# Kernel tuning notes

Measured on AMD Instinct MI355X. Metric: run time of the kernel, lower is better.

Reference implementation:

```python
import jax, jax.numpy as jnp
import numpy as np

DN = jax.lax.conv_dimension_numbers((1, 32, 32, 32, 1), (3, 3, 3, 1, 32), ('NDHWC', 'DHWIO', 'NDHWC'))


def setup_inputs() -> dict:
    key = jax.random.key(0)
    k0, k1, k2, k3, k4 = jax.random.split(key, 5)
    B = 64
    x = jax.random.normal(k0, (B, 32, 32, 32, 1), dtype=jnp.float32)
    # conv weights in DHWIO layout; kaiming-ish scale
    w1 = jax.random.normal(k1, (3, 3, 3, 1, 32), dtype=jnp.float32) * (1.0 / np.sqrt(27 * 1))
    b1 = jax.random.normal(k2, (32,), dtype=jnp.float32) * 0.01
    w2 = jax.random.normal(k3, (3, 3, 3, 32, 64), dtype=jnp.float32) * (1.0 / np.sqrt(27 * 32))
    b2 = jax.random.normal(k4, (64,), dtype=jnp.float32) * 0.01
    return {"x": x, "w1": w1, "b1": b1, "w2": w2, "b2": b2}


def _conv3d_valid(x, w):
    # x: [B, D, H, W, C_in], w: [kD, kH, kW, C_in, C_out] -> [B, D-2, H-2, W-2, C_out]
    dn = jax.lax.conv_dimension_numbers(x.shape, w.shape, ('NDHWC', 'DHWIO', 'NDHWC'))
    return jax.lax.conv_general_dilated(x, w, window_strides=(1, 1, 1),
                                        padding='VALID', dimension_numbers=dn)


def reference(x, w1, b1, w2, b2):
    # Dense input -> all voxels active, so spconv's gather-GEMM-scatter equals
    # a dense valid 3D conv. ReLU acts on active-site features == dense ReLU.
    h = jax.nn.relu(_conv3d_valid(x, w1) + b1)        # [B, 30, 30, 30, 32]
    h = jax.nn.relu(_conv3d_valid(h, w2) + b2)        # [B, 28, 28, 28, 64]
    # spconv ToDense returns NCDHW
    return jnp.transpose(h, (0, 4, 1, 2, 3))          # [B, 64, 28, 28, 28]
```

## Files before the change

kernel.cpp:

```cpp
#include <hip/hip_runtime.h>
#include <cstdint>
#include <cstddef>

typedef __attribute__((ext_vector_type(8))) short bf16x8;
typedef __attribute__((ext_vector_type(4))) float f32x4;
typedef __attribute__((ext_vector_type(4))) unsigned int u32x4;
typedef unsigned short u16;

#define H1_ROW_B   1920
#define H1_BATCH   (30 * 30 * 960)
#define LDS_STRIDE 1952
#define OUT_CSTR   21952

__device__ __forceinline__ u16 f2bf(float f) {
    union { float f; unsigned u; } v; v.f = f;
    unsigned r = v.u + 0x7FFF + ((v.u >> 16) & 1);
    return (u16)(r >> 16);
}

__device__ __forceinline__ void fma4(float4& a, float s, const float4& w) {
    a.x = fmaf(s, w.x, a.x);
    a.y = fmaf(s, w.y, a.y);
    a.z = fmaf(s, w.z, a.z);
    a.w = fmaf(s, w.w, a.w);
}

__global__ __launch_bounds__(256) void conv1_relu(
    const float* __restrict__ x, const float* __restrict__ w1,
    const float* __restrict__ b1, u16* __restrict__ h1, int b0)
{
    __shared__ float wl[27 * 32 + 32];

    const int z   = blockIdx.x;
    const int yt  = blockIdx.y;
    const int bl  = blockIdx.z;
    const int b   = b0 + bl;
    const int tid = threadIdx.x;

    for (int i = tid; i < 27 * 32; i += 256) wl[i] = w1[i];
    if (tid < 32) wl[27 * 32 + tid] = b1[tid];
    __syncthreads();

    const int c4   = tid & 7;
    const int slot = tid >> 3;

    const float4 bias = *reinterpret_cast<const float4*>(&wl[27 * 32 + c4 * 4]);
    const float* xb  = x + (size_t)b * 32768;
    u16*         h1b = h1 + (size_t)bl * H1_BATCH;

    if (slot < 30) {
#pragma unroll 1
        for (int j = 0; j < 3; ++j) {
            const int p  = slot + 30 * j;
            const int yy = p / 15;
            const int xx = (p - yy * 15) * 2;
            const int y  = yt * 6 + yy;

            float4 acc0 = bias, acc1 = bias;
#pragma unroll
            for (int kd = 0; kd < 3; ++kd) {
#pragma unroll
                for (int kh = 0; kh < 3; ++kh) {
                    const float* row = xb + ((size_t)(z + kd) * 32 + (y + kh)) * 32 + xx;
                    const float2 v01 = *reinterpret_cast<const float2*>(row);
                    const float2 v23 = *reinterpret_cast<const float2*>(row + 2);
                    const int t = (kd * 3 + kh) * 3;
                    const float4 w0  = *reinterpret_cast<const float4*>(&wl[(t + 0) * 32 + c4 * 4]);
                    const float4 w1v = *reinterpret_cast<const float4*>(&wl[(t + 1) * 32 + c4 * 4]);
                    const float4 w2v = *reinterpret_cast<const float4*>(&wl[(t + 2) * 32 + c4 * 4]);
                    fma4(acc0, v01.x, w0);
                    fma4(acc0, v01.y, w1v);
                    fma4(acc0, v23.x, w2v);
                    fma4(acc1, v01.y, w0);
                    fma4(acc1, v23.x, w1v);
                    fma4(acc1, v23.y, w2v);
                }
            }
            ushort4 s0, s1;
            s0.x = f2bf(fmaxf(acc0.x, 0.f)); s0.y = f2bf(fmaxf(acc0.y, 0.f));
            s0.z = f2bf(fmaxf(acc0.z, 0.f)); s0.w = f2bf(fmaxf(acc0.w, 0.f));
            s1.x = f2bf(fmaxf(acc1.x, 0.f)); s1.y = f2bf(fmaxf(acc1.y, 0.f));
            s1.z = f2bf(fmaxf(acc1.z, 0.f)); s1.w = f2bf(fmaxf(acc1.w, 0.f));
            u16* dst = h1b + ((size_t)(z * 30 + y) * 30 + xx) * 32 + c4 * 4;
            *reinterpret_cast<ushort4*>(dst)      = s0;
            *reinterpret_cast<ushort4*>(dst + 32) = s1;
        }
    }
}

__global__ __launch_bounds__(256) void pack_w2(
    const float* __restrict__ w2, u16* __restrict__ wB)
{
    const int tap = blockIdx.x;
    const int tid = threadIdx.x;
    const int nt = tid >> 6;
    const int l  = tid & 63;
    const int r = l & 15, q = l >> 4;
    u16* dst = wB + ((size_t)(tap * 4 + nt) * 64 + l) * 8;
#pragma unroll
    for (int j = 0; j < 8; ++j)
        dst[j] = f2bf(w2[(size_t)(tap * 32 + q * 8 + j) * 64 + nt * 16 + r]);
}

__global__ __launch_bounds__(256, 2) void conv2_mfma(
    const u16* __restrict__ h1, const u16* __restrict__ wB,
    const float* __restrict__ b2, float* __restrict__ out, int b0)
{
    __shared__ __align__(16) unsigned char smem[36 * LDS_STRIDE];

    const int g   = gridDim.x;
    const int bid = blockIdx.x;
    const int lb  = (g % 8 == 0) ? ((bid & 7) * (g >> 3) + (bid >> 3)) : bid;

    const int t0  = lb % 49;
    const int bl  = lb / 49;
    const int yg  = t0 % 7;
    const int zt  = t0 / 7;

    const int b  = b0 + bl;
    const int y0 = yg * 4, z0 = zt * 4;
    const int tid = threadIdx.x;
    const int wv  = tid >> 6;
    const int l   = tid & 63;
    const int r = l & 15, q = l >> 4;
    const int yl = r >> 2, xg = r & 3;

    const char* wBl = (const char*)wB + l * 16;

    {
        const char* gbase = (const char*)(h1 + (size_t)bl * H1_BATCH);
        for (int c = wv; c < 72; c += 4) {
            const int rid = c >> 1, half = c & 1;
            const int zz = rid / 6, yy = rid - zz * 6;
            const char* src = gbase
                + (size_t)((z0 + zz) * 30 + (y0 + yy)) * H1_ROW_B
                + half * 896 + l * 16;
            unsigned char* dst = smem + rid * LDS_STRIDE + half * 896 + l * 16;
            __builtin_amdgcn_global_load_lds(
                (const __attribute__((address_space(1))) void*)src,
                (__attribute__((address_space(3))) void*)dst, 16, 0, 0);
        }
    }
    __syncthreads();

    f32x4 acc[7][4];
    {
        const float bv0 = b2[r];
        const float bv1 = b2[16 + r];
        const float bv2 = b2[32 + r];
        const float bv3 = b2[48 + r];
#pragma unroll
        for (int mt = 0; mt < 7; ++mt) {
            acc[mt][0] = (f32x4){bv0, bv0, bv0, bv0};
            acc[mt][1] = (f32x4){bv1, bv1, bv1, bv1};
            acc[mt][2] = (f32x4){bv2, bv2, bv2, bv2};
            acc[mt][3] = (f32x4){bv3, bv3, bv3, bv3};
        }
    }

    const unsigned char* aBase =
        smem + (wv * 6 + yl) * LDS_STRIDE + xg * 64 + q * 16;

    u32x4 Bs[2][4];
#define B_LOAD(slot, t)                                                        \
    { const char* p_ = wBl + (size_t)(t) * 4096;                               \
      asm volatile("global_load_dwordx4 %0, %4, off\n\t"                       \
                   "global_load_dwordx4 %1, %4, off offset:1024\n\t"           \
                   "global_load_dwordx4 %2, %4, off offset:2048\n\t"           \
                   "global_load_dwordx4 %3, %4, off offset:3072"               \
                   : "=&v"(Bs[slot][0]), "=&v"(Bs[slot][1]),                   \
                     "=&v"(Bs[slot][2]), "=&v"(Bs[slot][3])                    \
                   : "v"(p_)); }

    B_LOAD(0, 0)

#pragma unroll
    for (int tap = 0; tap < 27; ++tap) {
        const int cur = tap & 1;

        if (tap < 26) B_LOAD(cur ^ 1, tap + 1)

        if (tap < 26) asm volatile("s_waitcnt vmcnt(4)");
        else          asm volatile("s_waitcnt vmcnt(0)");

        asm volatile("" : "+v"(Bs[cur][0]), "+v"(Bs[cur][1]),
                          "+v"(Bs[cur][2]), "+v"(Bs[cur][3]));
        const bf16x8 B0 = __builtin_bit_cast(bf16x8, Bs[cur][0]);
        const bf16x8 B1 = __builtin_bit_cast(bf16x8, Bs[cur][1]);
        const bf16x8 B2 = __builtin_bit_cast(bf16x8, Bs[cur][2]);
        const bf16x8 B3 = __builtin_bit_cast(bf16x8, Bs[cur][3]);

        const int kd = tap / 9;
        const int kh = (tap - kd * 9) / 3;
        const int kw = tap - kd * 9 - kh * 3;
        const unsigned char* ap = aBase + (kd * 6 + kh) * LDS_STRIDE + kw * 64;

        __builtin_amdgcn_s_setprio(1);
#pragma unroll
        for (int mt = 0; mt < 7; ++mt) {
            const bf16x8 a = *reinterpret_cast<const bf16x8*>(ap + mt * 256);
            acc[mt][0] = __builtin_amdgcn_mfma_f32_16x16x32_bf16(a, B0, acc[mt][0], 0, 0, 0);
            acc[mt][1] = __builtin_amdgcn_mfma_f32_16x16x32_bf16(a, B1, acc[mt][1], 0, 0, 0);
            acc[mt][2] = __builtin_amdgcn_mfma_f32_16x16x32_bf16(a, B2, acc[mt][2], 0, 0, 0);
            acc[mt][3] = __builtin_amdgcn_mfma_f32_16x16x32_bf16(a, B3, acc[mt][3], 0, 0, 0);
        }
        __builtin_amdgcn_s_setprio(0);
    }
#undef B_LOAD

    const int z = z0 + wv;
    float* ob = out + ((size_t)b * 64 + r) * OUT_CSTR
                    + (size_t)z * 784 + (size_t)(y0 + q) * 28;
#pragma unroll
    for (int mt = 0; mt < 7; ++mt) {
#pragma unroll
        for (int nt = 0; nt < 4; ++nt) {
            const f32x4 v = acc[mt][nt];
            float4 st;
            st.x = fmaxf(v.x, 0.f);
            st.y = fmaxf(v.y, 0.f);
            st.z = fmaxf(v.z, 0.f);
            st.w = fmaxf(v.w, 0.f);
            *reinterpret_cast<float4*>(ob + (size_t)nt * 16 * OUT_CSTR + mt * 4) = st;
        }
    }
}

extern "C" void kernel_launch(void* const* d_in, const int* in_sizes, int n_in,
                              void* d_out, int out_size, void* d_ws, size_t ws_size,
                              hipStream_t stream)
{
    const float* x  = (const float*)d_in[0];
    const float* w1 = (const float*)d_in[1];
    const float* b1 = (const float*)d_in[2];
    const float* w2 = (const float*)d_in[3];
    const float* b2 = (const float*)d_in[4];
    float* out = (float*)d_out;

    u16* wB = (u16*)d_ws;
    u16* h1 = (u16*)((char*)d_ws + 131072);

    pack_w2<<<27, 256, 0, stream>>>(w2, wB);

    const size_t per_batch = (size_t)H1_BATCH * 2;
    size_t avail = ws_size > 131072 ? ws_size - 131072 : 0;
    int bchunk = (int)(avail / per_batch);
    if (bchunk < 1)  bchunk = 1;
    if (bchunk > 64) bchunk = 64;

    for (int b0 = 0; b0 < 64; b0 += bchunk) {
        int bc = 64 - b0;
        if (bc > bchunk) bc = bchunk;
        conv1_relu<<<dim3(30, 5, bc), 256, 0, stream>>>(x, w1, b1, h1, b0);
        conv2_mfma<<<dim3(49 * bc), 256, 0, stream>>>(h1, wB, b2, out, b0);
    }
}
```

Measured before the change: 295.5 us.

## Split conv2 x-range across two waves per z-slice with 512-thread blocks

The conv2 MFMA kernel moves from 4 waves to 8 waves per block. Each z-slice's 7 M-tiles are now split between two waves, one taking 4 tiles and the other 3, with the compute body templated on tile count and x offset. The aim is more waves per block for better latency hiding and fewer accumulator registers per wave. In exchange, every B-weight load is duplicated across twice as many waves, and the two halves carry unequal work.

```diff
diff --git a/kernel.cpp b/kernel.cpp
--- a/kernel.cpp
+++ b/kernel.cpp
@@ -102,64 +102,26 @@
         dst[j] = f2bf(w2[(size_t)(tap * 32 + q * 8 + j) * 64 + nt * 16 + r]);
 }
 
-__global__ __launch_bounds__(256, 2) void conv2_mfma(
-    const u16* __restrict__ h1, const u16* __restrict__ wB,
-    const float* __restrict__ b2, float* __restrict__ out, int b0)
-{
-    __shared__ __align__(16) unsigned char smem[36 * LDS_STRIDE];
-
-    const int g   = gridDim.x;
-    const int bid = blockIdx.x;
-    const int lb  = (g % 8 == 0) ? ((bid & 7) * (g >> 3) + (bid >> 3)) : bid;
-
-    const int t0  = lb % 49;
-    const int bl  = lb / 49;
-    const int yg  = t0 % 7;
-    const int zt  = t0 / 7;
-
-    const int b  = b0 + bl;
-    const int y0 = yg * 4, z0 = zt * 4;
-    const int tid = threadIdx.x;
-    const int wv  = tid >> 6;
-    const int l   = tid & 63;
+template<int NMT, int XOUT>
+__device__ __forceinline__ void conv2_body(
+    const unsigned char* smem, const char* wBl,
+    const float* __restrict__ b2, float* __restrict__ out,
+    int b, int y0, int z0, int zw, int l)
+{
     const int r = l & 15, q = l >> 4;
     const int yl = r >> 2, xg = r & 3;
 
-    const char* wBl = (const char*)wB + l * 16;
-
-    {
-        const char* gbase = (const char*)(h1 + (size_t)bl * H1_BATCH);
-        for (int c = wv; c < 72; c += 4) {
-            const int rid = c >> 1, half = c & 1;
-            const int zz = rid / 6, yy = rid - zz * 6;
-            const char* src = gbase
-                + (size_t)((z0 + zz) * 30 + (y0 + yy)) * H1_ROW_B
-                + half * 896 + l * 16;
-            unsigned char* dst = smem + rid * LDS_STRIDE + half * 896 + l * 16;
-            __builtin_amdgcn_global_load_lds(
-                (const __attribute__((address_space(1))) void*)src,
-                (__attribute__((address_space(3))) void*)dst, 16, 0, 0);
-        }
-    }
-    __syncthreads();
-
-    f32x4 acc[7][4];
-    {
-        const float bv0 = b2[r];
-        const float bv1 = b2[16 + r];
-        const float bv2 = b2[32 + r];
-        const float bv3 = b2[48 + r];
-#pragma unroll
-        for (int mt = 0; mt < 7; ++mt) {
-            acc[mt][0] = (f32x4){bv0, bv0, bv0, bv0};
-            acc[mt][1] = (f32x4){bv1, bv1, bv1, bv1};
-            acc[mt][2] = (f32x4){bv2, bv2, bv2, bv2};
-            acc[mt][3] = (f32x4){bv3, bv3, bv3, bv3};
-        }
+    f32x4 acc[NMT][4];
+#pragma unroll
+    for (int nt = 0; nt < 4; ++nt) {
+        const float bv = b2[nt * 16 + r];
+        const f32x4 bi = {bv, bv, bv, bv};
+#pragma unroll
+        for (int mt = 0; mt < NMT; ++mt) acc[mt][nt] = bi;
     }
 
     const unsigned char* aBase =
-        smem + (wv * 6 + yl) * LDS_STRIDE + xg * 64 + q * 16;
+        smem + (zw * 6 + yl) * LDS_STRIDE + (XOUT + xg) * 64 + q * 16;
 
     u32x4 Bs[2][4];
 #define B_LOAD(slot, t)                                                        \
@@ -197,7 +159,7 @@
 
         __builtin_amdgcn_s_setprio(1);
 #pragma unroll
-        for (int mt = 0; mt < 7; ++mt) {
+        for (int mt = 0; mt < NMT; ++mt) {
             const bf16x8 a = *reinterpret_cast<const bf16x8*>(ap + mt * 256);
             acc[mt][0] = __builtin_amdgcn_mfma_f32_16x16x32_bf16(a, B0, acc[mt][0], 0, 0, 0);
             acc[mt][1] = __builtin_amdgcn_mfma_f32_16x16x32_bf16(a, B1, acc[mt][1], 0, 0, 0);
@@ -208,11 +170,11 @@
     }
 #undef B_LOAD
 
-    const int z = z0 + wv;
+    const int z = z0 + zw;
     float* ob = out + ((size_t)b * 64 + r) * OUT_CSTR
-                    + (size_t)z * 784 + (size_t)(y0 + q) * 28;
-#pragma unroll
-    for (int mt = 0; mt < 7; ++mt) {
+                    + (size_t)z * 784 + (size_t)(y0 + q) * 28 + XOUT;
+#pragma unroll
+    for (int mt = 0; mt < NMT; ++mt) {
 #pragma unroll
         for (int nt = 0; nt < 4; ++nt) {
             const f32x4 v = acc[mt][nt];
@@ -226,6 +188,53 @@
     }
 }
 
+__global__ __launch_bounds__(512, 4) void conv2_mfma(
+    const u16* __restrict__ h1, const u16* __restrict__ wB,
+    const float* __restrict__ b2, float* __restrict__ out, int b0)
+{
+    __shared__ __align__(16) unsigned char smem[36 * LDS_STRIDE];
+
+    const int g   = gridDim.x;
+    const int bid = blockIdx.x;
+    const int lb  = (g % 8 == 0) ? ((bid & 7) * (g >> 3) + (bid >> 3)) : bid;
+
+    const int t0  = lb % 49;
+    const int bl  = lb / 49;
+    const int yg  = t0 % 7;
+    const int zt  = t0 / 7;
+
+    const int b  = b0 + bl;
+    const int y0 = yg * 4, z0 = zt * 4;
+    const int tid = threadIdx.x;
+    const int wv  = tid >> 6;
+    const int l   = tid & 63;
+    const int zw  = wv >> 1;
+    const int xh  = wv & 1;
+
+    const char* wBl = (const char*)wB + l * 16;
+
+    {
+        const char* gbase = (const char*)(h1 + (size_t)bl * H1_BATCH);
+        for (int c = wv; c < 72; c += 8) {
+            const int rid = c >> 1, half = c & 1;
+            const int zz = rid / 6, yy = rid - zz * 6;
+            const char* src = gbase
+                + (size_t)((z0 + zz) * 30 + (y0 + yy)) * H1_ROW_B
+                + half * 896 + l * 16;
+            unsigned char* dst = smem + rid * LDS_STRIDE + half * 896 + l * 16;
+            __builtin_amdgcn_global_load_lds(
+                (const __attribute__((address_space(1))) void*)src,
+                (__attribute__((address_space(3))) void*)dst, 16, 0, 0);
+        }
+    }
+    __syncthreads();
+
+    if (xh == 0)
+        conv2_body<4, 0>(smem, wBl, b2, out, b, y0, z0, zw, l);
+    else
+        conv2_body<3, 16>(smem, wBl, b2, out, b, y0, z0, zw, l);
+}
+
 extern "C" void kernel_launch(void* const* d_in, const int* in_sizes, int n_in,
                               void* d_out, int out_size, void* d_ws, size_t ws_size,
                               hipStream_t stream)
@@ -252,6 +261,6 @@
         int bc = 64 - b0;
         if (bc > bchunk) bc = bchunk;
         conv1_relu<<<dim3(30, 5, bc), 256, 0, stream>>>(x, w1, b1, h1, b0);
-        conv2_mfma<<<dim3(49 * bc), 256, 0, stream>>>(h1, wB, b2, out, b0);
-    }
-}
+        conv2_mfma<<<dim3(49 * bc), 512, 0, stream>>>(h1, wB, b2, out, b0);
+    }
+}
```

Result: no change. 297.8 us (+0.8%).
